# Performance work log

Measured on AMD Instinct MI355X. Metric: run time of the kernel, lower is better.

Reference implementation:

```python
import jax, jax.numpy as jnp
import numpy as np

B, N, H, F = 4, 4096, 128, 64
ADJ_DENSITY = 0.01


def setup_inputs() -> dict:
    key = jax.random.key(0)
    k1, k2, k3, k4, k5 = jax.random.split(key, 5)
    x = jax.random.normal(k1, (B, N, H), dtype=jnp.float32)
    w_scale = jnp.float32(1.0 / np.sqrt(H))  # ~ nn.Linear init scale
    Wq = jax.random.normal(k2, (H, F), dtype=jnp.float32) * w_scale
    Wk = jax.random.normal(k3, (H, F), dtype=jnp.float32) * w_scale
    Wv = jax.random.normal(k4, (H, F), dtype=jnp.float32) * w_scale
    # Sparse binary adjacency with self-loops (every row has >=1 neighbor,
    # so no all--inf softmax rows).
    adj = (jax.random.uniform(k5, (N, N)) < ADJ_DENSITY).astype(jnp.float32)
    diag = jnp.arange(N)
    adj = adj.at[diag, diag].set(1.0)
    return {"x": x, "Wq": Wq, "Wk": Wk, "Wv": Wv, "adj": adj}


def reference(x, Wq, Wk, Wv, adj):
    # x: (B,N,H); Wq/Wk/Wv: (H,F); adj: (N,N) binary, broadcast over batch.
    q = x @ Wq  # (B,N,F)
    k = x @ Wk  # (B,N,F)
    v = x @ Wv  # (B,N,F)
    scale = jnp.float32(F) ** -0.5  # k.shape[-1] ** -0.5
    scores = jnp.einsum("bnf,bmf->bnm", q, k) * scale  # (B,N,N)
    scores = jnp.where(adj[None] == 0, -jnp.inf, scores)
    # softmax over neighbors, then the module adds the adjacency back (wei + adj)
    wei = jax.nn.softmax(scores, axis=-1) + adj[None]  # (B,N,N)
    # dropout is identity in eval/deterministic reference
    out = jnp.einsum("bnm,bmf->bnf", wei, v)  # (B,N,F)
    return out
```

## Files before the change

kernel.cpp:

```cpp
#include <hip/hip_runtime.h>
#include <math.h>

#define Bb 4
#define Nn 4096
#define Hh 128
#define Ff 64
#define CAP 128

typedef __attribute__((ext_vector_type(8))) short bf16x8;
typedef __attribute__((ext_vector_type(4))) float f32x4;

__device__ __forceinline__ unsigned short f2bf(float f) {
  unsigned int u = __float_as_uint(f);
  u += 0x7fffu + ((u >> 16) & 1u);
  return (unsigned short)(u >> 16);
}
__device__ __forceinline__ float bf2f(unsigned short h) {
  return __uint_as_float(((unsigned int)h) << 16);
}

__global__ __launch_bounds__(256) void qkv_kernel(
    const float* __restrict__ x,
    const float* __restrict__ Wq,
    const float* __restrict__ Wk,
    const float* __restrict__ Wv,
    float* __restrict__ q,
    unsigned short* __restrict__ kb,
    unsigned short* __restrict__ vb) {
  __shared__ short xs[64 * 128];

  const int tid = threadIdx.x;
  const int w = tid >> 6;
  const int lane = tid & 63;

  const int row0 = (int)blockIdx.x * 64;
  const int half = lane >> 4;
  const int l16 = lane & 15;

  const float4* xg = (const float4*)(x + (size_t)row0 * Hh);
#pragma unroll
  for (int j = 0; j < 8; ++j) {
    const int idx = tid + 256 * j;
    const int row = idx >> 5;
    const int c4 = idx & 31;
    const float4 xv = xg[idx];
    uint2 p;
    p.x = (unsigned)f2bf(xv.x) | ((unsigned)f2bf(xv.y) << 16);
    p.y = (unsigned)f2bf(xv.z) | ((unsigned)f2bf(xv.w) << 16);
    const int addr = (row * 256 + c4 * 8) ^ ((row & 7) << 4);
    *(uint2*)((char*)xs + addr) = p;
  }

  bf16x8 bfr[3][4];
#pragma unroll
  for (int nt = 0; nt < 3; ++nt) {
    const int n0g = w * 48 + nt * 16;
    const float* Wm = (n0g < 64) ? Wq : (n0g < 128) ? Wk : Wv;
    const int c0 = n0g & 63;
#pragma unroll
    for (int ks = 0; ks < 4; ++ks) {
      bf16x8 f;
#pragma unroll
      for (int j = 0; j < 8; ++j) {
        const int kr = ks * 32 + half * 8 + j;
        f[j] = (short)f2bf(Wm[kr * Ff + c0 + l16]);
      }
      bfr[nt][ks] = f;
    }
  }
  __syncthreads();

  f32x4 acc[4][3];
#pragma unroll
  for (int mt = 0; mt < 4; ++mt)
#pragma unroll
    for (int nt = 0; nt < 3; ++nt)
#pragma unroll
      for (int r = 0; r < 4; ++r) acc[mt][nt][r] = 0.f;

#pragma unroll
  for (int mt = 0; mt < 4; ++mt) {
    const int arow = mt * 16 + l16;
    const int abase = arow * 256;
    const int aswz = (arow & 7) << 4;
#pragma unroll
    for (int ks = 0; ks < 4; ++ks) {
      const int addr = (abase + ks * 64 + half * 16) ^ aswz;
      const bf16x8 a = *(const bf16x8*)((const char*)xs + addr);
#pragma unroll
      for (int nt = 0; nt < 3; ++nt) {
        acc[mt][nt] = __builtin_amdgcn_mfma_f32_16x16x32_bf16(
            a, bfr[nt][ks], acc[mt][nt], 0, 0, 0);
      }
    }
  }

#pragma unroll
  for (int mt = 0; mt < 4; ++mt) {
#pragma unroll
    for (int nt = 0; nt < 3; ++nt) {
      const int n0g = w * 48 + nt * 16;
      const int col = (n0g & 63) + l16;
#pragma unroll
      for (int r = 0; r < 4; ++r) {
        const size_t rowg = (size_t)row0 + mt * 16 + half * 4 + r;
        const float val = acc[mt][nt][r];
        if (n0g < 64)
          q[rowg * Ff + col] = val;
        else if (n0g < 128)
          kb[rowg * Ff + col] = f2bf(val);
        else
          vb[rowg * Ff + col] = f2bf(val);
      }
    }
  }
}

__global__ __launch_bounds__(256) void csr_kernel(
    const float* __restrict__ adj,
    unsigned short* __restrict__ g_nbr,
    int* __restrict__ g_cnt) {
  __shared__ __align__(8) unsigned short stg[4][CAP];

  const int tid = threadIdx.x;
  const int w = tid >> 6;
  const int lane = tid & 63;

  const int n = (int)blockIdx.x * 4 + w;
  const float* arow = adj + (size_t)n * Nn;

  ((ushort2*)stg[w])[lane] = make_ushort2(0, 0);

  float4 a4[16];
#pragma unroll
  for (int c = 0; c < 16; ++c) a4[c] = ((const float4*)arow)[c * 64 + lane];

  const unsigned long long ltmask =
      (lane == 0) ? 0ull : (~0ull >> (64 - lane));
  int off = 0;
#pragma unroll
  for (int c = 0; c < 16; ++c) {
#pragma unroll
    for (int comp = 0; comp < 4; ++comp) {
      const float val = comp == 0 ? a4[c].x
                      : comp == 1 ? a4[c].y
                      : comp == 2 ? a4[c].z
                                  : a4[c].w;
      const bool nz = (val != 0.f);
      const unsigned long long mm = __ballot(nz);
      if (nz) {
        const int pos = off + (int)__popcll(mm & ltmask);
        if (pos < CAP)
          stg[w][pos] = (unsigned short)(c * 256 + 4 * lane + comp);
      }
      off += (int)__popcll(mm);
    }
  }

  if (lane == 0) g_cnt[n] = off < CAP ? off : CAP;
  ((ushort2*)(g_nbr + (size_t)n * CAP))[lane] = ((const ushort2*)stg[w])[lane];
}

__global__ __launch_bounds__(256) void attn_kernel(
    const unsigned short* __restrict__ g_nbr,
    const int* __restrict__ g_cnt,
    const float* __restrict__ q,
    const unsigned short* __restrict__ kb,
    const unsigned short* __restrict__ vb,
    float* __restrict__ out) {
  __shared__ __align__(8) unsigned short nbr[CAP];
  __shared__ float qs[4][64];
  __shared__ float ps[4][64];

  const int n = blockIdx.x;
  const int tid = threadIdx.x;
  const int w = tid >> 6;
  const int lane = tid & 63;

  qs[w][lane] = q[((size_t)w * Nn + n) * Ff + lane];
  if (w == 0) {
    ((ushort2*)nbr)[lane] = ((const ushort2*)(g_nbr + (size_t)n * CAP))[lane];
  }
  const int tot = g_cnt[n];
  __syncthreads();

  const int b = w;
  const unsigned short* kbb = kb + (size_t)b * Nn * Ff;
  const unsigned short* vbb = vb + (size_t)b * Nn * Ff;

  const int g = lane >> 2;
  const int sl = lane & 3;

  float4 q0a = *(const float4*)&qs[b][8 * sl];
  float4 q0b = *(const float4*)&qs[b][8 * sl + 4];
  float4 q1a = *(const float4*)&qs[b][32 + 8 * sl];
  float4 q1b = *(const float4*)&qs[b][32 + 8 * sl + 4];

  float M = -INFINITY, L = 0.f, acc = 0.f, vsum = 0.f;

  const int ntiles = (tot + 63) >> 6;
  for (int t = 0; t < ntiles; ++t) {
    const int tbase = t << 6;

    float s0, s1, s2, s3;
#define BPAIR(u, qlo, qhi, a)                                   \
    {                                                           \
      const float flo = __uint_as_float((u) << 16);             \
      const float fhi = __uint_as_float((u) & 0xffff0000u);     \
      a = fmaf(qlo, flo, a);                                    \
      a = fmaf(qhi, fhi, a);                                    \
    }
#define DOT_ROW(i, sdst)                                                  \
    {                                                                     \
      const int idx = tbase + g + 16 * (i);                               \
      const bool valid = idx < tot;                                       \
      const int m = valid ? (int)nbr[idx] : 0;                            \
      const char* krow = (const char*)(kbb + (size_t)m * Ff);             \
      const uint4 k0 = *(const uint4*)(krow + 16 * sl);                   \
      const uint4 k1 = *(const uint4*)(krow + 64 + 16 * sl);              \
      float a = 0.f;                                                      \
      BPAIR(k0.x, q0a.x, q0a.y, a)                                        \
      BPAIR(k0.y, q0a.z, q0a.w, a)                                        \
      BPAIR(k0.z, q0b.x, q0b.y, a)                                        \
      BPAIR(k0.w, q0b.z, q0b.w, a)                                        \
      BPAIR(k1.x, q1a.x, q1a.y, a)                                        \
      BPAIR(k1.y, q1a.z, q1a.w, a)                                        \
      BPAIR(k1.z, q1b.x, q1b.y, a)                                        \
      BPAIR(k1.w, q1b.z, q1b.w, a)                                        \
      a += __shfl_xor(a, 1, 64);                                          \
      a += __shfl_xor(a, 2, 64);                                          \
      sdst = valid ? a * 0.125f : -INFINITY;                              \
    }
    DOT_ROW(0, s0)
    DOT_ROW(1, s1)
    DOT_ROW(2, s2)
    DOT_ROW(3, s3)
#undef DOT_ROW
#undef BPAIR

    float lm = fmaxf(fmaxf(s0, s1), fmaxf(s2, s3));
#pragma unroll
    for (int o = 32; o; o >>= 1) lm = fmaxf(lm, __shfl_xor(lm, o, 64));
    const float newM = fmaxf(M, lm);

    const float p0 = (s0 == -INFINITY) ? 0.f : __expf(s0 - newM);
    const float p1 = (s1 == -INFINITY) ? 0.f : __expf(s1 - newM);
    const float p2 = (s2 == -INFINITY) ? 0.f : __expf(s2 - newM);
    const float p3 = (s3 == -INFINITY) ? 0.f : __expf(s3 - newM);

    float psum = ((p0 + p1) + (p2 + p3));
#pragma unroll
    for (int o = 32; o >= 4; o >>= 1) psum += __shfl_xor(psum, o, 64);

    const float corr = __expf(M - newM);
    L = L * corr + psum;
    acc *= corr;
    M = newM;

    const float pw = sl == 0 ? p0 : sl == 1 ? p1 : sl == 2 ? p2 : p3;
    ps[w][g + 16 * sl] = pw;

    const int jmax = min(64, tot - tbase);
#pragma unroll 4
    for (int j = 0; j < jmax; ++j) {
      const int m = nbr[tbase + j];
      const float vf = bf2f(vbb[(size_t)m * Ff + lane]);
      acc = fmaf(ps[w][j], vf, acc);
      vsum += vf;
    }
  }

  out[((size_t)b * Nn + n) * Ff + lane] = acc / L + vsum;
}

extern "C" void kernel_launch(void* const* d_in, const int* in_sizes, int n_in,
                              void* d_out, int out_size, void* d_ws, size_t ws_size,
                              hipStream_t stream) {
  const float* x = (const float*)d_in[0];
  const float* Wq = (const float*)d_in[1];
  const float* Wk = (const float*)d_in[2];
  const float* Wv = (const float*)d_in[3];
  const float* adj = (const float*)d_in[4];
  float* out = (float*)d_out;

  char* ws = (char*)d_ws;
  const size_t rows = (size_t)Bb * Nn;
  float* q = (float*)ws;
  unsigned short* kb = (unsigned short*)(ws + rows * Ff * 4);
  unsigned short* vb = (unsigned short*)(ws + rows * Ff * 4 + rows * Ff * 2);
  unsigned short* g_nbr = (unsigned short*)(ws + rows * Ff * 8);
  int* g_cnt = (int*)(ws + rows * Ff * 8 + (size_t)Nn * CAP * 2);

  qkv_kernel<<<dim3(256), dim3(256), 0, stream>>>(x, Wq, Wk, Wv, q, kb, vb);
  csr_kernel<<<dim3(Nn / 4), dim3(256), 0, stream>>>(adj, g_nbr, g_cnt);
  attn_kernel<<<dim3(Nn), dim3(256), 0, stream>>>(g_nbr, g_cnt, q, kb, vb, out);
}
```

Baseline: 55.23 us.

## Fuse adjacency-row compaction into the attention kernel and drop the CSR pass

Removes the separate CSR kernel and has each attention block read its own adjacency row, count nonzeros per thread, run a wave and block prefix sum, and scatter neighbor indices into shared memory. This saves one kernel launch and the global write and read of the neighbor lists and counts. In exchange, the extra adjacency load and scan now sit at the start of every attention block before any attention work begins, and the neighbor cap is raised to 192.

```diff
diff --git a/kernel.cpp b/kernel.cpp
--- a/kernel.cpp
+++ b/kernel.cpp
@@ -5,7 +5,7 @@
 #define Nn 4096
 #define Hh 128
 #define Ff 64
-#define CAP 128
+#define NBR_CAP 192
 
 typedef __attribute__((ext_vector_type(8))) short bf16x8;
 typedef __attribute__((ext_vector_type(4))) float f32x4;
@@ -116,61 +116,16 @@
   }
 }
 
-__global__ __launch_bounds__(256) void csr_kernel(
+__global__ __launch_bounds__(256) void attn_kernel(
     const float* __restrict__ adj,
-    unsigned short* __restrict__ g_nbr,
-    int* __restrict__ g_cnt) {
-  __shared__ __align__(8) unsigned short stg[4][CAP];
-
-  const int tid = threadIdx.x;
-  const int w = tid >> 6;
-  const int lane = tid & 63;
-
-  const int n = (int)blockIdx.x * 4 + w;
-  const float* arow = adj + (size_t)n * Nn;
-
-  ((ushort2*)stg[w])[lane] = make_ushort2(0, 0);
-
-  float4 a4[16];
-#pragma unroll
-  for (int c = 0; c < 16; ++c) a4[c] = ((const float4*)arow)[c * 64 + lane];
-
-  const unsigned long long ltmask =
-      (lane == 0) ? 0ull : (~0ull >> (64 - lane));
-  int off = 0;
-#pragma unroll
-  for (int c = 0; c < 16; ++c) {
-#pragma unroll
-    for (int comp = 0; comp < 4; ++comp) {
-      const float val = comp == 0 ? a4[c].x
-                      : comp == 1 ? a4[c].y
-                      : comp == 2 ? a4[c].z
-                                  : a4[c].w;
-      const bool nz = (val != 0.f);
-      const unsigned long long mm = __ballot(nz);
-      if (nz) {
-        const int pos = off + (int)__popcll(mm & ltmask);
-        if (pos < CAP)
-          stg[w][pos] = (unsigned short)(c * 256 + 4 * lane + comp);
-      }
-      off += (int)__popcll(mm);
-    }
-  }
-
-  if (lane == 0) g_cnt[n] = off < CAP ? off : CAP;
-  ((ushort2*)(g_nbr + (size_t)n * CAP))[lane] = ((const ushort2*)stg[w])[lane];
-}
-
-__global__ __launch_bounds__(256) void attn_kernel(
-    const unsigned short* __restrict__ g_nbr,
-    const int* __restrict__ g_cnt,
     const float* __restrict__ q,
     const unsigned short* __restrict__ kb,
     const unsigned short* __restrict__ vb,
     float* __restrict__ out) {
-  __shared__ __align__(8) unsigned short nbr[CAP];
+  __shared__ __align__(8) unsigned short nbr[NBR_CAP];
   __shared__ float qs[4][64];
   __shared__ float ps[4][64];
+  __shared__ int wcnt[4];
 
   const int n = blockIdx.x;
   const int tid = threadIdx.x;
@@ -178,10 +133,53 @@
   const int lane = tid & 63;
 
   qs[w][lane] = q[((size_t)w * Nn + n) * Ff + lane];
-  if (w == 0) {
-    ((ushort2*)nbr)[lane] = ((const ushort2*)(g_nbr + (size_t)n * CAP))[lane];
-  }
-  const int tot = g_cnt[n];
+
+  const float* arow = adj + (size_t)n * Nn;
+  float4 a4[4];
+#pragma unroll
+  for (int j = 0; j < 4; ++j) a4[j] = ((const float4*)arow)[tid + 256 * j];
+
+  int cnt = 0;
+#pragma unroll
+  for (int j = 0; j < 4; ++j) {
+    cnt += (a4[j].x != 0.f) + (a4[j].y != 0.f) + (a4[j].z != 0.f) +
+           (a4[j].w != 0.f);
+  }
+
+  int inc = cnt;
+#pragma unroll
+  for (int o = 1; o < 64; o <<= 1) {
+    const int t = __shfl_up(inc, o, 64);
+    if (lane >= o) inc += t;
+  }
+  if (lane == 63) wcnt[w] = inc;
+  __syncthreads();
+
+  int base = 0, tot = 0;
+#pragma unroll
+  for (int w2 = 0; w2 < 4; ++w2) {
+    const int c = wcnt[w2];
+    if (w2 < w) base += c;
+    tot += c;
+  }
+  if (tot > NBR_CAP) tot = NBR_CAP;
+
+  int pos = base + (inc - cnt);
+#pragma unroll
+  for (int j = 0; j < 4; ++j) {
+    const int col0 = 4 * (tid + 256 * j);
+#pragma unroll
+    for (int comp = 0; comp < 4; ++comp) {
+      const float val = comp == 0 ? a4[j].x
+                      : comp == 1 ? a4[j].y
+                      : comp == 2 ? a4[j].z
+                                  : a4[j].w;
+      if (val != 0.f) {
+        if (pos < NBR_CAP) nbr[pos] = (unsigned short)(col0 + comp);
+        ++pos;
+      }
+    }
+  }
   __syncthreads();
 
   const int b = w;
@@ -288,10 +286,7 @@
   float* q = (float*)ws;
   unsigned short* kb = (unsigned short*)(ws + rows * Ff * 4);
   unsigned short* vb = (unsigned short*)(ws + rows * Ff * 4 + rows * Ff * 2);
-  unsigned short* g_nbr = (unsigned short*)(ws + rows * Ff * 8);
-  int* g_cnt = (int*)(ws + rows * Ff * 8 + (size_t)Nn * CAP * 2);
 
   qkv_kernel<<<dim3(256), dim3(256), 0, stream>>>(x, Wq, Wk, Wv, q, kb, vb);
-  csr_kernel<<<dim3(Nn / 4), dim3(256), 0, stream>>>(adj, g_nbr, g_cnt);
-  attn_kernel<<<dim3(Nn), dim3(256), 0, stream>>>(g_nbr, g_cnt, q, kb, vb, out);
-}
+  attn_kernel<<<dim3(Nn), dim3(256), 0, stream>>>(adj, q, kb, vb, out);
+}
```

New measurement: 50.06 us. 1.1x faster.
